# Performance work log

Hardware: AMD Instinct MI355X
Metric: run time of the kernel (lower is better)

## Reference

```python
import jax, jax.numpy as jnp
import numpy as np

NEG = -1000000000.0  # mask sentinel used by the torch module

def setup_inputs() -> dict:
    key = jax.random.key(0)
    k1, k2, k3, k4 = jax.random.split(key, 4)
    B, N, F_in, F_out = 8, 2048, 128, 64
    h = jax.random.normal(k1, (B, N, F_in), dtype=jnp.float32)
    adj_mask = jnp.where(jax.random.uniform(k2, (B, N, N)) < 0.7, 0.0, NEG).astype(jnp.float32)
    # xavier_uniform with gain=1.414
    g = 1.414
    limW = g * np.sqrt(6.0 / (F_in + F_out))
    W = jax.random.uniform(k3, (F_in, F_out), minval=-limW, maxval=limW, dtype=jnp.float32)
    lima = g * np.sqrt(6.0 / (2 * F_out + 1))
    a = jax.random.uniform(k4, (2 * F_out, 1), minval=-lima, maxval=lima, dtype=jnp.float32)
    return {"h": h, "adj_mask": adj_mask, "W": W, "a": a}

def reference(h, adj_mask, W, a):
    F_out = W.shape[1]
    wh = jnp.matmul(h, W)                       # [B, N, F_out]
    wh1 = jnp.matmul(wh, a[:F_out])             # [B, N, 1]
    wh2 = jnp.matmul(wh, a[F_out:])             # [B, N, 1]
    e = wh1 + jnp.swapaxes(wh2, 1, 2)           # [B, N, N] additive score
    e = jax.nn.leaky_relu(e, negative_slope=0.2)
    e = jnp.where(adj_mask == NEG, NEG, e)
    attention = jax.nn.softmax(e, axis=-1)      # dropout is identity in eval mode
    h_prime = jnp.matmul(attention, wh)         # [B, N, F_out]
    return jax.nn.elu(h_prime)
```

## Files before the change

### kernel.cpp

```cpp
#include <hip/hip_runtime.h>
#include <hip/hip_bf16.h>

#define BATCH 8
#define NN 2048
#define FIN 128
#define FOUT 64
#define ROWS_TOTAL (BATCH * NN)

typedef __attribute__((ext_vector_type(8))) short bf16x8;
typedef __attribute__((ext_vector_type(4))) float f32x4;
typedef __attribute__((ext_vector_type(8))) short short8;

__device__ inline short f2bf(float x) {
    __hip_bfloat16 b = __float2bfloat16(x);
    short s;
    __builtin_memcpy(&s, &b, 2);
    return s;
}

__device__ inline bf16x8 score8(float q, float4 w0, float4 w1, float4 a0, float4 a1) {
    float p[8];
    float e;
    e = q + w0.x; p[0] = __expf(fmaxf(e, 0.2f * e) + a0.x);
    e = q + w0.y; p[1] = __expf(fmaxf(e, 0.2f * e) + a0.y);
    e = q + w0.z; p[2] = __expf(fmaxf(e, 0.2f * e) + a0.z);
    e = q + w0.w; p[3] = __expf(fmaxf(e, 0.2f * e) + a0.w);
    e = q + w1.x; p[4] = __expf(fmaxf(e, 0.2f * e) + a1.x);
    e = q + w1.y; p[5] = __expf(fmaxf(e, 0.2f * e) + a1.y);
    e = q + w1.z; p[6] = __expf(fmaxf(e, 0.2f * e) + a1.z);
    e = q + w1.w; p[7] = __expf(fmaxf(e, 0.2f * e) + a1.w);
    bf16x8 r;
    #pragma unroll
    for (int i = 0; i < 8; ++i) r[i] = f2bf(p[i]);
    return r;
}

__global__ __launch_bounds__(256) void k1_proj(
        const float* __restrict__ h, const float* __restrict__ W,
        const float* __restrict__ a,
        short* __restrict__ whT, float* __restrict__ wh1, float* __restrict__ wh2) {
    const int tid  = threadIdx.x;
    const int lane = tid & 63;
    const int wid  = tid >> 6;
    const int gw   = blockIdx.x * 4 + wid;
    const int row0 = gw * 8;
    const int b    = row0 >> 11;
    const int rloc = row0 & (NN - 1);

    float acc[8] = {0.f,0.f,0.f,0.f,0.f,0.f,0.f,0.f};
    const float* hrow = h + (size_t)row0 * FIN;

    #pragma unroll 2
    for (int kc = 0; kc < FIN / 4; ++kc) {
        float wv0 = W[(4*kc + 0) * FOUT + lane];
        float wv1 = W[(4*kc + 1) * FOUT + lane];
        float wv2 = W[(4*kc + 2) * FOUT + lane];
        float wv3 = W[(4*kc + 3) * FOUT + lane];
        #pragma unroll
        for (int r = 0; r < 8; ++r) {
            float4 h4 = *(const float4*)(hrow + r * FIN + 4*kc);
            acc[r] = fmaf(h4.x, wv0, acc[r]);
            acc[r] = fmaf(h4.y, wv1, acc[r]);
            acc[r] = fmaf(h4.z, wv2, acc[r]);
            acc[r] = fmaf(h4.w, wv3, acc[r]);
        }
    }

    short8 st;
    #pragma unroll
    for (int r = 0; r < 8; ++r) st[r] = f2bf(acc[r]);
    *(short8*)(whT + ((size_t)b * FOUT + lane) * NN + rloc) = st;

    const float a1 = a[lane];
    const float a2 = a[FOUT + lane];
    #pragma unroll
    for (int r = 0; r < 8; ++r) {
        const int row = row0 + r;
        float v1 = acc[r] * a1;
        float v2 = acc[r] * a2;
        #pragma unroll
        for (int m = 32; m >= 1; m >>= 1) {
            v1 += __shfl_xor(v1, m, 64);
            v2 += __shfl_xor(v2, m, 64);
        }
        if (lane == 0) { wh1[row] = v1; wh2[row] = v2; }
    }
}

__global__ __launch_bounds__(512, 4) void k2_attn(
        const float* __restrict__ adj, const short* __restrict__ whT,
        const float* __restrict__ wh1, const float* __restrict__ wh2,
        float* __restrict__ out) {
    __shared__ float lds_acc[8][16][FOUT];
    __shared__ float lds_l[8][16];

    const int tid  = threadIdx.x;
    const int lane = tid & 63;
    const int w    = tid >> 6;
    const int row0 = blockIdx.x * 16;
    const int b    = row0 >> 11;
    const int iloc = lane & 15;
    const int koff = (lane >> 4) * 8;

    const float* adjrow = adj + (size_t)(row0 + iloc) * NN;
    const float* wh2b   = wh2 + b * NN;
    const short* whTb   = whT + (size_t)b * FOUT * NN;
    const float  wh1v   = wh1[row0 + iloc];

    bf16x8 onesf, idxf;
    #pragma unroll
    for (int e = 0; e < 8; ++e) { onesf[e] = (short)0x3F80; idxf[e] = f2bf((float)iloc); }
    f32x4 rowM = {}, colM = {};
    rowM = __builtin_amdgcn_mfma_f32_16x16x32_bf16(idxf, onesf, rowM, 0, 0, 0);
    colM = __builtin_amdgcn_mfma_f32_16x16x32_bf16(onesf, idxf, colM, 0, 0, 0);
    int rmap[4], cmap[4];
    #pragma unroll
    for (int reg = 0; reg < 4; ++reg) {
        int r = (int)(rowM[reg] * 0.03125f + 0.5f);
        int c = (int)(colM[reg] * 0.03125f + 0.5f);
        rmap[reg] = min(max(r, 0), 15);
        cmap[reg] = min(max(c, 0), 15);
    }

    f32x4 acc[4] = {};
    f32x4 accl = {};

    const int base = w * 32 + koff;

    float4 a0 = *(const float4*)(adjrow + base);
    float4 a1 = *(const float4*)(adjrow + base + 4);
    float4 w0 = *(const float4*)(wh2b + base);
    float4 w1 = *(const float4*)(wh2b + base + 4);

    #pragma unroll
    for (int k = 0; k < 8; ++k) {
        const int j0 = base + k * 256;

        bf16x8 bf[4];
        #pragma unroll
        for (int ft = 0; ft < 4; ++ft)
            bf[ft] = *(const bf16x8*)(whTb + (size_t)(ft * 16 + iloc) * NN + j0);

        float4 na0 = a0, na1 = a1, nw0 = w0, nw1 = w1;
        if (k < 7) {
            na0 = *(const float4*)(adjrow + j0 + 256);
            na1 = *(const float4*)(adjrow + j0 + 260);
            nw0 = *(const float4*)(wh2b + j0 + 256);
            nw1 = *(const float4*)(wh2b + j0 + 260);
        }

        bf16x8 af = score8(wh1v, w0, w1, a0, a1);

        accl = __builtin_amdgcn_mfma_f32_16x16x32_bf16(af, onesf, accl, 0, 0, 0);
        #pragma unroll
        for (int ft = 0; ft < 4; ++ft)
            acc[ft] = __builtin_amdgcn_mfma_f32_16x16x32_bf16(af, bf[ft], acc[ft], 0, 0, 0);

        a0 = na0; a1 = na1; w0 = nw0; w1 = nw1;
    }

    #pragma unroll
    for (int ft = 0; ft < 4; ++ft)
        #pragma unroll
        for (int reg = 0; reg < 4; ++reg)
            lds_acc[w][rmap[reg]][ft * 16 + cmap[reg]] = acc[ft][reg];
    #pragma unroll
    for (int reg = 0; reg < 4; ++reg)
        if (cmap[reg] == 0) lds_l[w][rmap[reg]] = accl[reg];
    __syncthreads();

    const int f  = tid & 63;
    const int rh = tid >> 6;
    #pragma unroll
    for (int rr = 0; rr < 2; ++rr) {
        const int r = rh * 2 + rr;
        float s = 0.f, l = 0.f;
        #pragma unroll
        for (int ww = 0; ww < 8; ++ww) {
            s += lds_acc[ww][r][f];
            l += lds_l[ww][r];
        }
        float v = s / l;
        out[(size_t)(row0 + r) * FOUT + f] = (v > 0.f) ? v : (__expf(v) - 1.f);
    }
}

extern "C" void kernel_launch(void* const* d_in, const int* in_sizes, int n_in,
                              void* d_out, int out_size, void* d_ws, size_t ws_size,
                              hipStream_t stream) {
    const float* h   = (const float*)d_in[0];
    const float* adj = (const float*)d_in[1];
    const float* W   = (const float*)d_in[2];
    const float* a   = (const float*)d_in[3];
    float* out = (float*)d_out;

    short* whT = (short*)d_ws;
    float* wh1 = (float*)(whT + (size_t)BATCH * FOUT * NN);
    float* wh2 = wh1 + ROWS_TOTAL;

    k1_proj<<<ROWS_TOTAL / 32, 256, 0, stream>>>(h, W, a, whT, wh1, wh2);
    k2_attn<<<ROWS_TOTAL / 16, 512, 0, stream>>>(adj, whT, wh1, wh2, out);
}
```

Before: 75.02 us.

## Stage adjacency tiles into LDS with async global_load_lds double buffering

Replaces the per-lane register prefetch of adjacency rows with a double-buffered LDS pipeline. Each 256-column chunk is loaded with global_load_lds in 16-byte units under an XOR swizzle, and a barrier is placed on every chunk. The aim is fully coalesced, asynchronous streaming of the large adj matrix while the current chunk is scored, in place of scattered 32-byte per-lane loads. The cost is added __syncthreads, LDS traffic and a removed occupancy hint in launch_bounds. Reads of the wh2 and whT chunks are no longer prefetched.

```diff
diff --git a/kernel.cpp b/kernel.cpp
--- a/kernel.cpp
+++ b/kernel.cpp
@@ -6,6 +6,8 @@
 #define FIN 128
 #define FOUT 64
 #define ROWS_TOTAL (BATCH * NN)
+#define JB 256
+#define NCH (NN / JB)
 
 typedef __attribute__((ext_vector_type(8))) short bf16x8;
 typedef __attribute__((ext_vector_type(4))) float f32x4;
@@ -87,11 +89,11 @@
     }
 }
 
-__global__ __launch_bounds__(512, 4) void k2_attn(
+__global__ __launch_bounds__(512) void k2_attn(
         const float* __restrict__ adj, const short* __restrict__ whT,
         const float* __restrict__ wh1, const float* __restrict__ wh2,
         float* __restrict__ out) {
-    __shared__ float lds_acc[8][16][FOUT];
+    __shared__ char smem[2 * 16 * JB * 4];
     __shared__ float lds_l[8][16];
 
     const int tid  = threadIdx.x;
@@ -100,12 +102,11 @@
     const int row0 = blockIdx.x * 16;
     const int b    = row0 >> 11;
     const int iloc = lane & 15;
-    const int koff = (lane >> 4) * 8;
-
-    const float* adjrow = adj + (size_t)(row0 + iloc) * NN;
-    const float* wh2b   = wh2 + b * NN;
-    const short* whTb   = whT + (size_t)b * FOUT * NN;
-    const float  wh1v   = wh1[row0 + iloc];
+    const int kg   = lane >> 4;
+
+    const float* wh2b = wh2 + b * NN;
+    const short* whTb = whT + (size_t)b * FOUT * NN;
+    const float  wh1v = wh1[row0 + iloc];
 
     bf16x8 onesf, idxf;
     #pragma unroll
@@ -125,45 +126,67 @@
     f32x4 acc[4] = {};
     f32x4 accl = {};
 
-    const int base = w * 32 + koff;
-
-    float4 a0 = *(const float4*)(adjrow + base);
-    float4 a1 = *(const float4*)(adjrow + base + 4);
-    float4 w0 = *(const float4*)(wh2b + base);
-    float4 w1 = *(const float4*)(wh2b + base + 4);
-
-    #pragma unroll
-    for (int k = 0; k < 8; ++k) {
-        const int j0 = base + k * 256;
+    const int s0 = tid;
+    const int s1 = 512 + tid;
+    const int r0s = s0 >> 6, c0s = s0 & 63;
+    const int r1s = s1 >> 6, c1s = s1 & 63;
+    const float* src0base = adj + (size_t)(row0 + r0s) * NN + ((c0s ^ (r0s & 7)) << 2);
+    const float* src1base = adj + (size_t)(row0 + r1s) * NN + ((c1s ^ (r1s & 7)) << 2);
+
+    #define STAGE(chunk, bufsel)                                                   \
+        do {                                                                       \
+            char* dst = smem + (bufsel) * (16 * JB * 4);                           \
+            __builtin_amdgcn_global_load_lds(                                      \
+                (const __attribute__((address_space(1))) unsigned int*)(src0base + (size_t)(chunk) * JB), \
+                (__attribute__((address_space(3))) unsigned int*)(dst + s0 * 16),  \
+                16, 0, 0);                                                         \
+            __builtin_amdgcn_global_load_lds(                                      \
+                (const __attribute__((address_space(1))) unsigned int*)(src1base + (size_t)(chunk) * JB), \
+                (__attribute__((address_space(3))) unsigned int*)(dst + s1 * 16),  \
+                16, 0, 0);                                                         \
+        } while (0)
+
+    const int cpr = w * 8 + kg * 2;
+    const int swz = iloc & 7;
+    const int rd0 = iloc * (JB * 4) + ((cpr ^ swz) << 4);
+    const int rd1 = iloc * (JB * 4) + (((cpr + 1) ^ swz) << 4);
+
+    STAGE(0, 0);
+
+    for (int cn = 0; cn < NCH; ++cn) {
+        __syncthreads();
+        if (cn < NCH - 1) STAGE(cn + 1, (cn + 1) & 1);
+
+        const char* bufc = smem + (cn & 1) * (16 * JB * 4);
+        float4 a0 = *(const float4*)(bufc + rd0);
+        float4 a1 = *(const float4*)(bufc + rd1);
+
+        const int j0 = cn * JB + w * 32 + kg * 8;
+        float4 w0 = *(const float4*)(wh2b + j0);
+        float4 w1 = *(const float4*)(wh2b + j0 + 4);
 
         bf16x8 bf[4];
         #pragma unroll
         for (int ft = 0; ft < 4; ++ft)
             bf[ft] = *(const bf16x8*)(whTb + (size_t)(ft * 16 + iloc) * NN + j0);
 
-        float4 na0 = a0, na1 = a1, nw0 = w0, nw1 = w1;
-        if (k < 7) {
-            na0 = *(const float4*)(adjrow + j0 + 256);
-            na1 = *(const float4*)(adjrow + j0 + 260);
-            nw0 = *(const float4*)(wh2b + j0 + 256);
-            nw1 = *(const float4*)(wh2b + j0 + 260);
-        }
-
         bf16x8 af = score8(wh1v, w0, w1, a0, a1);
 
         accl = __builtin_amdgcn_mfma_f32_16x16x32_bf16(af, onesf, accl, 0, 0, 0);
         #pragma unroll
         for (int ft = 0; ft < 4; ++ft)
             acc[ft] = __builtin_amdgcn_mfma_f32_16x16x32_bf16(af, bf[ft], acc[ft], 0, 0, 0);
-
-        a0 = na0; a1 = na1; w0 = nw0; w1 = nw1;
-    }
-
+    }
+    #undef STAGE
+
+    __syncthreads();
+
+    float* lds_acc = (float*)smem;
     #pragma unroll
     for (int ft = 0; ft < 4; ++ft)
         #pragma unroll
         for (int reg = 0; reg < 4; ++reg)
-            lds_acc[w][rmap[reg]][ft * 16 + cmap[reg]] = acc[ft][reg];
+            lds_acc[(w * 16 + rmap[reg]) * FOUT + ft * 16 + cmap[reg]] = acc[ft][reg];
     #pragma unroll
     for (int reg = 0; reg < 4; ++reg)
         if (cmap[reg] == 0) lds_l[w][rmap[reg]] = accl[reg];
@@ -177,7 +200,7 @@
         float s = 0.f, l = 0.f;
         #pragma unroll
         for (int ww = 0; ww < 8; ++ww) {
-            s += lds_acc[ww][r][f];
+            s += lds_acc[(ww * 16 + r) * FOUT + f];
             l += lds_l[ww][r];
         }
         float v = s / l;
```

New measurement: 70.70 us (median of 2 runs). 1.06x faster.

## Compress adjacency mask to bitmask in projection kernel, consume bits in attention

Applied to the files above, without the earlier changes.

Adds a second role to the projection kernel: extra blocks read the fp32 adjacency matrix and ballot it into a 64-bit-per-word bitmask, which the attention kernel loads into LDS and uses to zero masked exponentials. The adjacency is still read once in full, so this mainly restructures where that read happens and lets the projection and mask passes run in the same launch. The attention kernel's per-iteration traffic shrinks from fp32 mask values to bits. The cost is an extra global write and read of the bitmask, and the removal of the explicit prefetch and the occupancy hint. Masked entries become exact zeros rather than exp(-1e9), which behaves the same unless a whole row is masked.

```diff
diff --git a/kernel.cpp b/kernel.cpp
--- a/kernel.cpp
+++ b/kernel.cpp
@@ -6,6 +6,10 @@
 #define FIN 128
 #define FOUT 64
 #define ROWS_TOTAL (BATCH * NN)
+#define K1_BLOCKS 512
+#define K0_BLOCKS 2048
+#define K0_WAVES (K0_BLOCKS * 4)
+#define MASK_WORDS (ROWS_TOTAL * (NN / 64))
 
 typedef __attribute__((ext_vector_type(8))) short bf16x8;
 typedef __attribute__((ext_vector_type(4))) float f32x4;
@@ -18,79 +22,76 @@
     return s;
 }
 
-__device__ inline bf16x8 score8(float q, float4 w0, float4 w1, float4 a0, float4 a1) {
-    float p[8];
-    float e;
-    e = q + w0.x; p[0] = __expf(fmaxf(e, 0.2f * e) + a0.x);
-    e = q + w0.y; p[1] = __expf(fmaxf(e, 0.2f * e) + a0.y);
-    e = q + w0.z; p[2] = __expf(fmaxf(e, 0.2f * e) + a0.z);
-    e = q + w0.w; p[3] = __expf(fmaxf(e, 0.2f * e) + a0.w);
-    e = q + w1.x; p[4] = __expf(fmaxf(e, 0.2f * e) + a1.x);
-    e = q + w1.y; p[5] = __expf(fmaxf(e, 0.2f * e) + a1.y);
-    e = q + w1.z; p[6] = __expf(fmaxf(e, 0.2f * e) + a1.z);
-    e = q + w1.w; p[7] = __expf(fmaxf(e, 0.2f * e) + a1.w);
-    bf16x8 r;
-    #pragma unroll
-    for (int i = 0; i < 8; ++i) r[i] = f2bf(p[i]);
-    return r;
-}
-
-__global__ __launch_bounds__(256) void k1_proj(
+__global__ __launch_bounds__(256) void k01(
         const float* __restrict__ h, const float* __restrict__ W,
-        const float* __restrict__ a,
-        short* __restrict__ whT, float* __restrict__ wh1, float* __restrict__ wh2) {
+        const float* __restrict__ a, const float* __restrict__ adj,
+        short* __restrict__ whT, float* __restrict__ wh1, float* __restrict__ wh2,
+        unsigned long long* __restrict__ maskg) {
     const int tid  = threadIdx.x;
     const int lane = tid & 63;
     const int wid  = tid >> 6;
-    const int gw   = blockIdx.x * 4 + wid;
-    const int row0 = gw * 8;
-    const int b    = row0 >> 11;
-    const int rloc = row0 & (NN - 1);
-
-    float acc[8] = {0.f,0.f,0.f,0.f,0.f,0.f,0.f,0.f};
-    const float* hrow = h + (size_t)row0 * FIN;
-
-    #pragma unroll 2
-    for (int kc = 0; kc < FIN / 4; ++kc) {
-        float wv0 = W[(4*kc + 0) * FOUT + lane];
-        float wv1 = W[(4*kc + 1) * FOUT + lane];
-        float wv2 = W[(4*kc + 2) * FOUT + lane];
-        float wv3 = W[(4*kc + 3) * FOUT + lane];
+
+    if (blockIdx.x < K1_BLOCKS) {
+        const int gw   = blockIdx.x * 4 + wid;
+        const int row0 = gw * 8;
+        const int b    = row0 >> 11;
+        const int rloc = row0 & (NN - 1);
+
+        float acc[8] = {0.f,0.f,0.f,0.f,0.f,0.f,0.f,0.f};
+        const float* hrow = h + (size_t)row0 * FIN;
+
+        #pragma unroll 2
+        for (int kc = 0; kc < FIN / 4; ++kc) {
+            float wv0 = W[(4*kc + 0) * FOUT + lane];
+            float wv1 = W[(4*kc + 1) * FOUT + lane];
+            float wv2 = W[(4*kc + 2) * FOUT + lane];
+            float wv3 = W[(4*kc + 3) * FOUT + lane];
+            #pragma unroll
+            for (int r = 0; r < 8; ++r) {
+                float4 h4 = *(const float4*)(hrow + r * FIN + 4*kc);
+                acc[r] = fmaf(h4.x, wv0, acc[r]);
+                acc[r] = fmaf(h4.y, wv1, acc[r]);
+                acc[r] = fmaf(h4.z, wv2, acc[r]);
+                acc[r] = fmaf(h4.w, wv3, acc[r]);
+            }
+        }
+
+        short8 st;
+        #pragma unroll
+        for (int r = 0; r < 8; ++r) st[r] = f2bf(acc[r]);
+        *(short8*)(whT + ((size_t)b * FOUT + lane) * NN + rloc) = st;
+
+        const float a1 = a[lane];
+        const float a2 = a[FOUT + lane];
         #pragma unroll
         for (int r = 0; r < 8; ++r) {
-            float4 h4 = *(const float4*)(hrow + r * FIN + 4*kc);
-            acc[r] = fmaf(h4.x, wv0, acc[r]);
-            acc[r] = fmaf(h4.y, wv1, acc[r]);
-            acc[r] = fmaf(h4.z, wv2, acc[r]);
-            acc[r] = fmaf(h4.w, wv3, acc[r]);
-        }
-    }
-
-    short8 st;
-    #pragma unroll
-    for (int r = 0; r < 8; ++r) st[r] = f2bf(acc[r]);
-    *(short8*)(whT + ((size_t)b * FOUT + lane) * NN + rloc) = st;
-
-    const float a1 = a[lane];
-    const float a2 = a[FOUT + lane];
-    #pragma unroll
-    for (int r = 0; r < 8; ++r) {
-        const int row = row0 + r;
-        float v1 = acc[r] * a1;
-        float v2 = acc[r] * a2;
-        #pragma unroll
-        for (int m = 32; m >= 1; m >>= 1) {
-            v1 += __shfl_xor(v1, m, 64);
-            v2 += __shfl_xor(v2, m, 64);
-        }
-        if (lane == 0) { wh1[row] = v1; wh2[row] = v2; }
-    }
-}
-
-__global__ __launch_bounds__(512, 4) void k2_attn(
-        const float* __restrict__ adj, const short* __restrict__ whT,
+            const int row = row0 + r;
+            float v1 = acc[r] * a1;
+            float v2 = acc[r] * a2;
+            #pragma unroll
+            for (int m = 32; m >= 1; m >>= 1) {
+                v1 += __shfl_xor(v1, m, 64);
+                v2 += __shfl_xor(v2, m, 64);
+            }
+            if (lane == 0) { wh1[row] = v1; wh2[row] = v2; }
+        }
+    } else {
+        const int gw = (blockIdx.x - K1_BLOCKS) * 4 + wid;
+        #pragma unroll 4
+        for (int it = 0; it < MASK_WORDS / K0_WAVES; ++it) {
+            const size_t wd = (size_t)it * K0_WAVES + gw;
+            float v = adj[wd * 64 + lane];
+            unsigned long long m = __ballot(v == 0.0f);
+            if (lane == 0) maskg[wd] = m;
+        }
+    }
+}
+
+__global__ __launch_bounds__(512) void k2_attn(
+        const unsigned long long* __restrict__ maskg, const short* __restrict__ whT,
         const float* __restrict__ wh1, const float* __restrict__ wh2,
         float* __restrict__ out) {
+    __shared__ unsigned long long lds_mask64[512];
     __shared__ float lds_acc[8][16][FOUT];
     __shared__ float lds_l[8][16];
 
@@ -100,12 +101,13 @@
     const int row0 = blockIdx.x * 16;
     const int b    = row0 >> 11;
     const int iloc = lane & 15;
-    const int koff = (lane >> 4) * 8;
-
-    const float* adjrow = adj + (size_t)(row0 + iloc) * NN;
-    const float* wh2b   = wh2 + b * NN;
-    const short* whTb   = whT + (size_t)b * FOUT * NN;
-    const float  wh1v   = wh1[row0 + iloc];
+    const int kg   = lane >> 4;
+
+    const float* wh2b = wh2 + b * NN;
+    const short* whTb = whT + (size_t)b * FOUT * NN;
+    const float  wh1v = wh1[row0 + iloc];
+
+    lds_mask64[tid] = maskg[(size_t)row0 * 32 + tid];
 
     bf16x8 onesf, idxf;
     #pragma unroll
@@ -122,41 +124,46 @@
         cmap[reg] = min(max(c, 0), 15);
     }
 
+    __syncthreads();
+    const unsigned char* mb8 = (const unsigned char*)lds_mask64;
+
     f32x4 acc[4] = {};
     f32x4 accl = {};
 
-    const int base = w * 32 + koff;
-
-    float4 a0 = *(const float4*)(adjrow + base);
-    float4 a1 = *(const float4*)(adjrow + base + 4);
-    float4 w0 = *(const float4*)(wh2b + base);
-    float4 w1 = *(const float4*)(wh2b + base + 4);
-
-    #pragma unroll
-    for (int k = 0; k < 8; ++k) {
-        const int j0 = base + k * 256;
+    #pragma unroll 2
+    for (int cn = 0; cn < 8; ++cn) {
+        const int j0 = cn * 256 + w * 32 + kg * 8;
+
+        const unsigned int mb = mb8[iloc * 256 + cn * 32 + w * 4 + kg];
+
+        float4 w0 = *(const float4*)(wh2b + j0);
+        float4 w1 = *(const float4*)(wh2b + j0 + 4);
 
         bf16x8 bf[4];
         #pragma unroll
         for (int ft = 0; ft < 4; ++ft)
             bf[ft] = *(const bf16x8*)(whTb + (size_t)(ft * 16 + iloc) * NN + j0);
 
-        float4 na0 = a0, na1 = a1, nw0 = w0, nw1 = w1;
-        if (k < 7) {
-            na0 = *(const float4*)(adjrow + j0 + 256);
-            na1 = *(const float4*)(adjrow + j0 + 260);
-            nw0 = *(const float4*)(wh2b + j0 + 256);
-            nw1 = *(const float4*)(wh2b + j0 + 260);
-        }
-
-        bf16x8 af = score8(wh1v, w0, w1, a0, a1);
+        float pv[8];
+        {
+            float e, pe;
+            e = wh1v + w0.x; pe = __expf(fmaxf(e, 0.2f*e)); pv[0] = (mb & 1u)   ? pe : 0.f;
+            e = wh1v + w0.y; pe = __expf(fmaxf(e, 0.2f*e)); pv[1] = (mb & 2u)   ? pe : 0.f;
+            e = wh1v + w0.z; pe = __expf(fmaxf(e, 0.2f*e)); pv[2] = (mb & 4u)   ? pe : 0.f;
+            e = wh1v + w0.w; pe = __expf(fmaxf(e, 0.2f*e)); pv[3] = (mb & 8u)   ? pe : 0.f;
+            e = wh1v + w1.x; pe = __expf(fmaxf(e, 0.2f*e)); pv[4] = (mb & 16u)  ? pe : 0.f;
+            e = wh1v + w1.y; pe = __expf(fmaxf(e, 0.2f*e)); pv[5] = (mb & 32u)  ? pe : 0.f;
+            e = wh1v + w1.z; pe = __expf(fmaxf(e, 0.2f*e)); pv[6] = (mb & 64u)  ? pe : 0.f;
+            e = wh1v + w1.w; pe = __expf(fmaxf(e, 0.2f*e)); pv[7] = (mb & 128u) ? pe : 0.f;
+        }
+        bf16x8 af;
+        #pragma unroll
+        for (int e = 0; e < 8; ++e) af[e] = f2bf(pv[e]);
 
         accl = __builtin_amdgcn_mfma_f32_16x16x32_bf16(af, onesf, accl, 0, 0, 0);
         #pragma unroll
         for (int ft = 0; ft < 4; ++ft)
             acc[ft] = __builtin_amdgcn_mfma_f32_16x16x32_bf16(af, bf[ft], acc[ft], 0, 0, 0);
-
-        a0 = na0; a1 = na1; w0 = nw0; w1 = nw1;
     }
 
     #pragma unroll
@@ -197,7 +204,8 @@
     short* whT = (short*)d_ws;
     float* wh1 = (float*)(whT + (size_t)BATCH * FOUT * NN);
     float* wh2 = wh1 + ROWS_TOTAL;
-
-    k1_proj<<<ROWS_TOTAL / 32, 256, 0, stream>>>(h, W, a, whT, wh1, wh2);
-    k2_attn<<<ROWS_TOTAL / 16, 512, 0, stream>>>(adj, whT, wh1, wh2, out);
-}
+    unsigned long long* maskg = (unsigned long long*)(wh2 + ROWS_TOTAL);
+
+    k01<<<K1_BLOCKS + K0_BLOCKS, 256, 0, stream>>>(h, W, a, adj, whT, wh1, wh2, maskg);
+    k2_attn<<<ROWS_TOTAL / 16, 512, 0, stream>>>(maskg, whT, wh1, wh2, out);
+}
```

Result: slower. 105.7 us (+40.9%).
